# Optimization experiments

Measured on AMD Instinct MI355X. Metric: run time of the kernel, lower is better.

Reference implementation:

```python
import jax, jax.numpy as jnp
import numpy as np

PH, PW = 7, 7          # pooled output size
SR = 2                 # sampling_ratio (fixed grid per bin)
SCALE = 0.0625         # spatial_scale = 1/16


def _axis(v, size):
    """Per-axis bilinear setup, faithful to the original clamping logic.
    v: [K] float sample coords. Returns lo, hi int indices, frac l, 1-l, valid mask."""
    valid = (v >= -1.0) & (v <= size)
    vc = jnp.maximum(v, 0.0)
    lo0 = jnp.floor(vc).astype(jnp.int32)
    at_edge = lo0 >= size - 1
    lo = jnp.where(at_edge, size - 1, lo0)
    hi = jnp.where(at_edge, size - 1, lo0 + 1)
    vc = jnp.where(at_edge, jnp.asarray(size - 1, vc.dtype), vc)
    l = vc - lo.astype(vc.dtype)
    return lo, hi, l, 1.0 - l, valid


def roi_align(feat, rois):
    B, C, H, W = feat.shape
    feat_flat = feat.reshape(B, C, H * W)
    grid = (jnp.arange(SR, dtype=feat.dtype) + 0.5) / SR  # sub-bin offsets

    def per_roi(roi):
        b = roi[0].astype(jnp.int32)
        sw, sh = roi[1] * SCALE, roi[2] * SCALE
        ew, eh = roi[3] * SCALE, roi[4] * SCALE
        rw = jnp.maximum(ew - sw, 1.0)
        rh = jnp.maximum(eh - sh, 1.0)
        bh, bw = rh / PH, rw / PW
        # sample coordinates: y[PH,SR], x[PW,SR]
        y = sh + jnp.arange(PH, dtype=feat.dtype)[:, None] * bh + grid[None, :] * bh
        x = sw + jnp.arange(PW, dtype=feat.dtype)[:, None] * bw + grid[None, :] * bw
        y_lo, y_hi, ly, hy, vy = _axis(y.reshape(-1), H)  # [PH*SR]
        x_lo, x_hi, lx, hx, vx = _axis(x.reshape(-1), W)  # [PW*SR]
        valid = (vy[:, None] & vx[None, :]).astype(feat.dtype)  # out-of-range -> zero contribution
        w1 = hy[:, None] * hx[None, :] * valid
        w2 = hy[:, None] * lx[None, :] * valid
        w3 = ly[:, None] * hx[None, :] * valid
        w4 = ly[:, None] * lx[None, :] * valid
        i1 = y_lo[:, None] * W + x_lo[None, :]
        i2 = y_lo[:, None] * W + x_hi[None, :]
        i3 = y_hi[:, None] * W + x_lo[None, :]
        i4 = y_hi[:, None] * W + x_hi[None, :]
        fb = jnp.take(feat_flat, b, axis=0)  # [C, H*W]
        # gather + weighted sum -> [C, PH*SR, PW*SR]
        s = (jnp.take(fb, i1, axis=1) * w1 + jnp.take(fb, i2, axis=1) * w2
             + jnp.take(fb, i3, axis=1) * w3 + jnp.take(fb, i4, axis=1) * w4)
        # average over the SR x SR sampling grid per bin (== / count)
        return s.reshape(C, PH, SR, PW, SR).mean(axis=(2, 4))  # [C, PH, PW]

    return jax.vmap(per_roi)(rois)  # [N, C, PH, PW]


def setup_inputs() -> dict:
    key = jax.random.key(0)
    k1, k2, k3, k4, k5 = jax.random.split(key, 5)
    bottom_data = jax.random.normal(k1, (1, 1024, 50, 50), dtype=jnp.float32)
    n_rois, img = 512, 800.0
    x1 = jax.random.uniform(k2, (n_rois,), minval=0.0, maxval=img - 64.0)
    y1 = jax.random.uniform(k3, (n_rois,), minval=0.0, maxval=img - 64.0)
    bw = jax.random.uniform(k4, (n_rois,), minval=32.0, maxval=256.0)
    bh = jax.random.uniform(k5, (n_rois,), minval=32.0, maxval=256.0)
    x2 = jnp.minimum(x1 + bw, img)
    y2 = jnp.minimum(y1 + bh, img)
    bottom_rois = jnp.stack([jnp.zeros((n_rois,)), x1, y1, x2, y2], axis=1).astype(jnp.float32)
    return {"bottom_data": bottom_data, "bottom_rois": bottom_rois}


def reference(bottom_data, bottom_rois):
    return roi_align(bottom_data, bottom_rois)
```

## Files before the change

### kernel.cpp

```cpp
#include <hip/hip_runtime.h>

#define PH 7
#define PW 7
#define SCALE 0.0625f
#define C_TOTAL 1024
#define H_ 50
#define W_ 50
#define HW_TOTAL (H_ * W_)
#define NROIS 512
#define NBIN (PH * PW)
#define CHB 64
#define NCHUNK (C_TOTAL / CHB)
#define ROWB (W_ * C_TOTAL * 4)
#define COLB (C_TOTAL * 4)
#define RMAX 17
#define GP   65

#define TBL_OFF    (HW_TOTAL * C_TOTAL)
#define TBL_STRIDE 512

__global__ __launch_bounds__(256) void transpose_kernel(
    const float* __restrict__ feat, float* __restrict__ featT,
    const float* __restrict__ rois)
{
    __shared__ float tile[64][65];
    const int hw0 = (blockIdx.x % 40) * 64;
    const int c0  = (blockIdx.x / 40) * 64;
    const int tx = threadIdx.x & 63;
    const int ty = threadIdx.x >> 6;

    const int hw_r = hw0 + tx;
    if (hw_r < HW_TOTAL) {
        #pragma unroll
        for (int j = 0; j < 16; ++j) {
            const int c_l = j * 4 + ty;
            tile[c_l][tx] = feat[(size_t)(c0 + c_l) * HW_TOTAL + hw_r];
        }
    }
    __syncthreads();
    #pragma unroll
    for (int j = 0; j < 16; ++j) {
        const int hw_l = j * 4 + ty;
        const int hw = hw0 + hw_l;
        if (hw < HW_TOTAL)
            featT[(size_t)hw * C_TOTAL + c0 + tx] = tile[tx][hw_l];
    }

    const int roi_id = blockIdx.x;
    if (roi_id >= NROIS) return;
    const float* roi = rois + roi_id * 5;
    float* tbl  = featT + TBL_OFF + (size_t)roi_id * TBL_STRIDE;
    int*   tbli = (int*)tbl;
    const int tid = threadIdx.x;

    const float shy = roi[2] * SCALE, ehy = roi[4] * SCALE;
    const float rht = fmaxf(ehy - shy, 1.0f);
    const float bh  = rht * (1.0f / 7.0f);
    int r0 = (int)floorf(fmaxf(shy + 0.25f * bh, 0.0f));
    if (r0 > H_ - 1) r0 = H_ - 1;
    const int lol = (int)floorf(fmaxf(shy + 6.75f * bh, 0.0f));
    int r1 = (lol >= H_ - 1) ? (H_ - 1) : (lol + 1);
    if (r1 - r0 + 1 > RMAX) r1 = r0 + RMAX - 1;
    const int R  = r1 - r0 + 1;

    if (tid == 128) { tbli[456] = r0; tbli[457] = R; }

    if (tid < 7) {
        const float swx = roi[1] * SCALE, ewx = roi[3] * SCALE;
        const float rwd = fmaxf(ewx - swx, 1.0f);
        const float bw  = rwd * (1.0f / 7.0f);
        const float base = swx + (float)tid * bw;
        const float v0 = base + 0.25f * bw;
        const float v1 = base + 0.75f * bw;

        int lo0, hi0, lo1, hi1;
        float l0, h0, l1, h1, m0, m1;
        {
            const bool val = (v0 >= -1.0f) && (v0 <= (float)W_);
            float vc = fmaxf(v0, 0.0f);
            int lo = (int)floorf(vc);
            if (lo >= W_ - 1) { lo0 = W_ - 1; hi0 = W_ - 1; vc = (float)(W_ - 1); }
            else              { lo0 = lo; hi0 = lo + 1; }
            l0 = vc - (float)lo0; h0 = 1.0f - l0;
            m0 = val ? 1.0f : 0.0f;
        }
        {
            const bool val = (v1 >= -1.0f) && (v1 <= (float)W_);
            float vc = fmaxf(v1, 0.0f);
            int lo = (int)floorf(vc);
            if (lo >= W_ - 1) { lo1 = W_ - 1; hi1 = W_ - 1; vc = (float)(W_ - 1); }
            else              { lo1 = lo; hi1 = lo + 1; }
            l1 = vc - (float)lo1; h1 = 1.0f - l1;
            m1 = val ? 1.0f : 0.0f;
        }

        float W0 = h0 * m0, W1 = l0 * m0, W2 = h1 * m1, W3 = l1 * m1;
        int I0 = lo0, I1 = hi0, I2 = lo1, I3 = hi1;
        if (I1 == I0) { W0 += W1; W1 = 0.0f; }
        if (I2 == I0) { W0 += W2; W2 = 0.0f; }
        else if (I2 == I1) { W1 += W2; W2 = 0.0f; }
        if (I3 == I0) { W0 += W3; W3 = 0.0f; }
        else if (I3 == I1) { W1 += W3; W3 = 0.0f; }
        else if (I3 == I2) { W2 += W3; W3 = 0.0f; }

        #define CSH(A, B) if (W##A == 0.0f && W##B != 0.0f) { W##A = W##B; I##A = I##B; W##B = 0.0f; }
        CSH(0,1) CSH(1,2) CSH(2,3)
        CSH(0,1) CSH(1,2) CSH(2,3)
        CSH(0,1) CSH(1,2) CSH(2,3)
        #undef CSH

        tbli[tid * 4 + 0] = I0 * COLB; tbli[tid * 4 + 1] = I1 * COLB;
        tbli[tid * 4 + 2] = I2 * COLB; tbli[tid * 4 + 3] = I3 * COLB;
        tbl[32 + tid * 4 + 0] = W0; tbl[32 + tid * 4 + 1] = W1;
        tbl[32 + tid * 4 + 2] = W2; tbl[32 + tid * 4 + 3] = W3;
    }

    if (tid >= 64 && tid < 64 + NBIN) {
        const int bin = tid - 64;
        const int py  = bin / 7, px = bin - py * 7;
        const float base = shy + (float)py * bh;
        const float v0 = base + 0.25f * bh;
        const float v1 = base + 0.75f * bh;

        int lo0, hi0, lo1, hi1;
        float l0, h0, l1, h1, m0, m1;
        {
            const bool val = (v0 >= -1.0f) && (v0 <= (float)H_);
            float vc = fmaxf(v0, 0.0f);
            int lo = (int)floorf(vc);
            if (lo >= H_ - 1) { lo0 = H_ - 1; hi0 = H_ - 1; vc = (float)(H_ - 1); }
            else              { lo0 = lo; hi0 = lo + 1; }
            l0 = vc - (float)lo0; h0 = 1.0f - l0;
            m0 = val ? 0.25f : 0.0f;
        }
        {
            const bool val = (v1 >= -1.0f) && (v1 <= (float)H_);
            float vc = fmaxf(v1, 0.0f);
            int lo = (int)floorf(vc);
            if (lo >= H_ - 1) { lo1 = H_ - 1; hi1 = H_ - 1; vc = (float)(H_ - 1); }
            else              { lo1 = lo; hi1 = lo + 1; }
            l1 = vc - (float)lo1; h1 = 1.0f - l1;
            m1 = val ? 0.25f : 0.0f;
        }

        const int s0 = min(lo0 - r0, RMAX - 1), s1 = min(hi0 - r0, RMAX - 1);
        const int s2 = min(lo1 - r0, RMAX - 1), s3 = min(hi1 - r0, RMAX - 1);
        tbli[64 + 0 * NBIN + bin] = (s0 * 7 + px) * GP;
        tbli[64 + 1 * NBIN + bin] = (s1 * 7 + px) * GP;
        tbli[64 + 2 * NBIN + bin] = (s2 * 7 + px) * GP;
        tbli[64 + 3 * NBIN + bin] = (s3 * 7 + px) * GP;
        tbl[260 + 0 * NBIN + bin] = h0 * m0; tbl[260 + 1 * NBIN + bin] = l0 * m0;
        tbl[260 + 2 * NBIN + bin] = h1 * m1; tbl[260 + 3 * NBIN + bin] = l1 * m1;
    }
}

__device__ __forceinline__ float ldf(const char* base, unsigned byte_off) {
    return *reinterpret_cast<const float*>(base + byte_off);
}

__global__ __launch_bounds__(512, 6) void roi_sep_kernel(
    const float* __restrict__ featT,
    float* __restrict__ out)
{
    __shared__ __align__(16) float s_G[RMAX * 7 * GP];
    __shared__ __align__(16) float s_ytbl[392];

    const int blk    = blockIdx.x;
    const int roi_id = blk >> 4;
    const int chunk  = blk & (NCHUNK - 1);
    const int tid    = threadIdx.x;

    const float* tbl  = featT + TBL_OFF + (size_t)roi_id * TBL_STRIDE;
    const int*   tbli = (const int*)tbl;

    if (tid < 392) s_ytbl[tid] = tbl[64 + tid];

    const int r0 = __builtin_amdgcn_readfirstlane(tbli[456]);
    const int R  = __builtin_amdgcn_readfirstlane(tbli[457]);

    int   xo_s[7][4];
    float xw_s[7][4];
    #pragma unroll
    for (int i = 0; i < 7; ++i) {
        const int4   t = ((const int4*)tbli)[i];
        const float4 w = ((const float4*)tbl)[8 + i];
        xo_s[i][0] = __builtin_amdgcn_readfirstlane(t.x);
        xo_s[i][1] = __builtin_amdgcn_readfirstlane(t.y);
        xo_s[i][2] = __builtin_amdgcn_readfirstlane(t.z);
        xo_s[i][3] = __builtin_amdgcn_readfirstlane(t.w);
        xw_s[i][0] = __uint_as_float(__builtin_amdgcn_readfirstlane(__float_as_uint(w.x)));
        xw_s[i][1] = __uint_as_float(__builtin_amdgcn_readfirstlane(__float_as_uint(w.y)));
        xw_s[i][2] = __uint_as_float(__builtin_amdgcn_readfirstlane(__float_as_uint(w.z)));
        xw_s[i][3] = __uint_as_float(__builtin_amdgcn_readfirstlane(__float_as_uint(w.w)));
    }

    const int wave = tid >> 6, lane = tid & 63;
    const char* fb  = (const char*)featT;
    const int laneB = (chunk * CHB + lane) * 4;

    for (int rs = wave; rs < R; rs += 8) {
        const unsigned rb = (unsigned)(laneB + (r0 + rs) * ROWB);
        float f[7][4];
        #pragma unroll
        for (int px = 0; px < 7; ++px) {
            f[px][0] = ldf(fb + xo_s[px][0], rb);
            f[px][1] = ldf(fb + xo_s[px][1], rb);
            f[px][2] = ldf(fb + xo_s[px][2], rb);
            f[px][3] = ldf(fb + xo_s[px][3], rb);
        }
        __asm__ __volatile__("" ::: "memory");
        float* gbase = &s_G[rs * 7 * GP + lane];
        #pragma unroll
        for (int px = 0; px < 7; ++px) {
            gbase[px * GP] = (xw_s[px][0] * f[px][0] + xw_s[px][1] * f[px][1])
                           + (xw_s[px][2] * f[px][2] + xw_s[px][3] * f[px][3]);
        }
    }
    __syncthreads();

    const int* s_yi = (const int*)s_ytbl;
    const float* s_yw = s_ytbl + 196;
    float* obase = out + (size_t)roi_id * (C_TOTAL * NBIN)
                       + (size_t)chunk * CHB * NBIN;
    #pragma unroll
    for (int q = 0; q < 3; ++q) {
        const int o   = tid + (q << 9);
        const int c   = o / NBIN;
        const int bin = o - c * NBIN;
        const int i0 = s_yi[0 * NBIN + bin], i1 = s_yi[1 * NBIN + bin];
        const int i2 = s_yi[2 * NBIN + bin], i3 = s_yi[3 * NBIN + bin];
        const float w0 = s_yw[0 * NBIN + bin], w1 = s_yw[1 * NBIN + bin];
        const float w2 = s_yw[2 * NBIN + bin], w3 = s_yw[3 * NBIN + bin];
        const float a0 = (w0 * s_G[i0 + c]      + w1 * s_G[i1 + c])
                       + (w2 * s_G[i2 + c]      + w3 * s_G[i3 + c]);
        const float a1 = (w0 * s_G[i0 + c + 32] + w1 * s_G[i1 + c + 32])
                       + (w2 * s_G[i2 + c + 32] + w3 * s_G[i3 + c + 32]);
        __builtin_nontemporal_store(a0, obase + o);
        __builtin_nontemporal_store(a1, obase + o + 1568);
    }
    if (tid < 32) {
        const int o   = tid + 1536;
        const int c   = 31;
        const int bin = o - c * NBIN;
        const int i0 = s_yi[0 * NBIN + bin], i1 = s_yi[1 * NBIN + bin];
        const int i2 = s_yi[2 * NBIN + bin], i3 = s_yi[3 * NBIN + bin];
        const float w0 = s_yw[0 * NBIN + bin], w1 = s_yw[1 * NBIN + bin];
        const float w2 = s_yw[2 * NBIN + bin], w3 = s_yw[3 * NBIN + bin];
        const float a0 = (w0 * s_G[i0 + c]      + w1 * s_G[i1 + c])
                       + (w2 * s_G[i2 + c]      + w3 * s_G[i3 + c]);
        const float a1 = (w0 * s_G[i0 + c + 32] + w1 * s_G[i1 + c + 32])
                       + (w2 * s_G[i2 + c + 32] + w3 * s_G[i3 + c + 32]);
        __builtin_nontemporal_store(a0, obase + o);
        __builtin_nontemporal_store(a1, obase + o + 1568);
    }
}

__global__ __launch_bounds__(256) void roi_align_fallback(
    const float* __restrict__ feat,
    const float* __restrict__ rois,
    float* __restrict__ out)
{
    __shared__ float s_w[16][NBIN];
    __shared__ int   s_i[16][NBIN];

    const int blk    = blockIdx.x;
    const int roi_id = blk >> 3;
    const int chunk  = blk & 7;
    const int tid    = threadIdx.x;

    const float* roi = rois + roi_id * 5;

    if (tid < NBIN * 4) {
        const float swx = roi[1] * SCALE;
        const float shy = roi[2] * SCALE;
        const float ewx = roi[3] * SCALE;
        const float ehy = roi[4] * SCALE;
        const float rw = fmaxf(ewx - swx, 1.0f);
        const float rh = fmaxf(ehy - shy, 1.0f);
        const float bw = rw * (1.0f / PW);
        const float bh = rh * (1.0f / PH);

        const int bin = tid >> 2;
        const int s   = tid & 3;
        const int iy  = s >> 1, ix = s & 1;
        const int py  = bin / PW, px = bin % PW;

        const float y = shy + ((float)py + ((float)iy + 0.5f) * 0.5f) * bh;
        const float x = swx + ((float)px + ((float)ix + 0.5f) * 0.5f) * bw;

        const bool vy = (y >= -1.0f) && (y <= (float)H_);
        float yc = fmaxf(y, 0.0f);
        int ylo = (int)floorf(yc);
        int yhi;
        if (ylo >= H_ - 1) { ylo = H_ - 1; yhi = H_ - 1; yc = (float)(H_ - 1); }
        else               { yhi = ylo + 1; }
        const float ly = yc - (float)ylo;
        const float hy = 1.0f - ly;

        const bool vx = (x >= -1.0f) && (x <= (float)W_);
        float xc = fmaxf(x, 0.0f);
        int xlo = (int)floorf(xc);
        int xhi;
        if (xlo >= W_ - 1) { xlo = W_ - 1; xhi = W_ - 1; xc = (float)(W_ - 1); }
        else               { xhi = xlo + 1; }
        const float lx = xc - (float)xlo;
        const float hx = 1.0f - lx;

        const float v = (vy && vx) ? 0.25f : 0.0f;

        const int r = s * 4;
        s_w[r + 0][bin] = hy * hx * v;
        s_w[r + 1][bin] = hy * lx * v;
        s_w[r + 2][bin] = ly * hx * v;
        s_w[r + 3][bin] = ly * lx * v;
        s_i[r + 0][bin] = ylo * W_ + xlo;
        s_i[r + 1][bin] = ylo * W_ + xhi;
        s_i[r + 2][bin] = yhi * W_ + xlo;
        s_i[r + 3][bin] = yhi * W_ + xhi;
    }
    __syncthreads();

    const float* fbase = feat + (size_t)chunk * 128 * HW_TOTAL;
    float* obase = out + (size_t)roi_id * (C_TOTAL * NBIN)
                       + (size_t)chunk * 128 * NBIN;

    for (int o = tid; o < 128 * NBIN; o += 256) {
        const int c   = o / NBIN;
        const int bin = o - c * NBIN;
        const float* f = fbase + c * HW_TOTAL;
        float acc = 0.0f;
        #pragma unroll
        for (int r = 0; r < 16; ++r) acc += s_w[r][bin] * f[s_i[r][bin]];
        obase[o] = acc;
    }
}

extern "C" void kernel_launch(void* const* d_in, const int* in_sizes, int n_in,
                              void* d_out, int out_size, void* d_ws, size_t ws_size,
                              hipStream_t stream) {
    const float* feat = (const float*)d_in[0];
    const float* rois = (const float*)d_in[1];
    float* out = (float*)d_out;

    const size_t need = (size_t)(TBL_OFF + NROIS * TBL_STRIDE) * sizeof(float);
    if (ws_size >= need) {
        float* featT = (float*)d_ws;
        transpose_kernel<<<dim3(40 * (C_TOTAL / 64)), dim3(256), 0, stream>>>(feat, featT, rois);
        roi_sep_kernel<<<dim3(NROIS * NCHUNK), dim3(512), 0, stream>>>(featT, out);
    } else {
        roi_align_fallback<<<dim3(NROIS * 8), dim3(256), 0, stream>>>(feat, rois, out);
    }
}
```

Before: 48.34 us.

## Stage ROI output in LDS and write with vectorized nontemporal stores

Changes the per-bin y-table to an interleaved layout so each bin's four indices and weights load as one 16-byte LDS read. The y-interpolation phase now has each wave compute a range of bins for all 64 channels, writing results into a new shared staging buffer, followed by a barrier and a float4 nontemporal copy to global memory. This is meant to cut scalar LDS table reads and replace scalar global stores with wide stores. It adds about 12.5 KB of LDS per block, which may reduce occupancy, plus an extra barrier. The staging writes at stride NBIN may also cause bank conflicts.

Result: slower. 50.63 us (+4.7%).

```diff
diff --git a/kernel.cpp b/kernel.cpp
--- a/kernel.cpp
+++ b/kernel.cpp
@@ -16,6 +16,8 @@
 #define RMAX 17
 #define GP   65
 
+typedef float vf4 __attribute__((ext_vector_type(4)));
+
 #define TBL_OFF    (HW_TOTAL * C_TOTAL)
 #define TBL_STRIDE 512
 
@@ -145,12 +147,12 @@
 
         const int s0 = min(lo0 - r0, RMAX - 1), s1 = min(hi0 - r0, RMAX - 1);
         const int s2 = min(lo1 - r0, RMAX - 1), s3 = min(hi1 - r0, RMAX - 1);
-        tbli[64 + 0 * NBIN + bin] = (s0 * 7 + px) * GP;
-        tbli[64 + 1 * NBIN + bin] = (s1 * 7 + px) * GP;
-        tbli[64 + 2 * NBIN + bin] = (s2 * 7 + px) * GP;
-        tbli[64 + 3 * NBIN + bin] = (s3 * 7 + px) * GP;
-        tbl[260 + 0 * NBIN + bin] = h0 * m0; tbl[260 + 1 * NBIN + bin] = l0 * m0;
-        tbl[260 + 2 * NBIN + bin] = h1 * m1; tbl[260 + 3 * NBIN + bin] = l1 * m1;
+        tbli[64 + bin * 4 + 0] = (s0 * 7 + px) * GP;
+        tbli[64 + bin * 4 + 1] = (s1 * 7 + px) * GP;
+        tbli[64 + bin * 4 + 2] = (s2 * 7 + px) * GP;
+        tbli[64 + bin * 4 + 3] = (s3 * 7 + px) * GP;
+        tbl[260 + bin * 4 + 0] = h0 * m0; tbl[260 + bin * 4 + 1] = l0 * m0;
+        tbl[260 + bin * 4 + 2] = h1 * m1; tbl[260 + bin * 4 + 3] = l1 * m1;
     }
 }
 
@@ -164,6 +166,7 @@
 {
     __shared__ __align__(16) float s_G[RMAX * 7 * GP];
     __shared__ __align__(16) float s_ytbl[392];
+    __shared__ __align__(16) float s_st[CHB * NBIN];
 
     const int blk    = blockIdx.x;
     const int roi_id = blk >> 4;
@@ -218,41 +221,23 @@
     }
     __syncthreads();
 
-    const int* s_yi = (const int*)s_ytbl;
-    const float* s_yw = s_ytbl + 196;
+    const int bstart = (wave * NBIN) >> 3;
+    const int bend   = ((wave + 1) * NBIN) >> 3;
+    for (int bin = bstart; bin < bend; ++bin) {
+        const int4   yi = *(const int4*)  &s_ytbl[bin * 4];
+        const float4 yw = *(const float4*)&s_ytbl[196 + bin * 4];
+        const float acc = (yw.x * s_G[yi.x + lane] + yw.y * s_G[yi.y + lane])
+                        + (yw.z * s_G[yi.z + lane] + yw.w * s_G[yi.w + lane]);
+        s_st[lane * NBIN + bin] = acc;
+    }
+    __syncthreads();
+
     float* obase = out + (size_t)roi_id * (C_TOTAL * NBIN)
                        + (size_t)chunk * CHB * NBIN;
-    #pragma unroll
-    for (int q = 0; q < 3; ++q) {
-        const int o   = tid + (q << 9);
-        const int c   = o / NBIN;
-        const int bin = o - c * NBIN;
-        const int i0 = s_yi[0 * NBIN + bin], i1 = s_yi[1 * NBIN + bin];
-        const int i2 = s_yi[2 * NBIN + bin], i3 = s_yi[3 * NBIN + bin];
-        const float w0 = s_yw[0 * NBIN + bin], w1 = s_yw[1 * NBIN + bin];
-        const float w2 = s_yw[2 * NBIN + bin], w3 = s_yw[3 * NBIN + bin];
-        const float a0 = (w0 * s_G[i0 + c]      + w1 * s_G[i1 + c])
-                       + (w2 * s_G[i2 + c]      + w3 * s_G[i3 + c]);
-        const float a1 = (w0 * s_G[i0 + c + 32] + w1 * s_G[i1 + c + 32])
-                       + (w2 * s_G[i2 + c + 32] + w3 * s_G[i3 + c + 32]);
-        __builtin_nontemporal_store(a0, obase + o);
-        __builtin_nontemporal_store(a1, obase + o + 1568);
-    }
-    if (tid < 32) {
-        const int o   = tid + 1536;
-        const int c   = 31;
-        const int bin = o - c * NBIN;
-        const int i0 = s_yi[0 * NBIN + bin], i1 = s_yi[1 * NBIN + bin];
-        const int i2 = s_yi[2 * NBIN + bin], i3 = s_yi[3 * NBIN + bin];
-        const float w0 = s_yw[0 * NBIN + bin], w1 = s_yw[1 * NBIN + bin];
-        const float w2 = s_yw[2 * NBIN + bin], w3 = s_yw[3 * NBIN + bin];
-        const float a0 = (w0 * s_G[i0 + c]      + w1 * s_G[i1 + c])
-                       + (w2 * s_G[i2 + c]      + w3 * s_G[i3 + c]);
-        const float a1 = (w0 * s_G[i0 + c + 32] + w1 * s_G[i1 + c + 32])
-                       + (w2 * s_G[i2 + c + 32] + w3 * s_G[i3 + c + 32]);
-        __builtin_nontemporal_store(a0, obase + o);
-        __builtin_nontemporal_store(a1, obase + o + 1568);
-    }
+    const vf4* st4 = (const vf4*)s_st;
+    vf4* o4 = (vf4*)obase;
+    for (int q = tid; q < (CHB * NBIN) / 4; q += 512)
+        __builtin_nontemporal_store(st4[q], o4 + q);
 }
 
 __global__ __launch_bounds__(256) void roi_align_fallback(
```
